# Kernel optimization log

Measured on AMD Instinct MI355X. Metric: run time of the kernel, lower is better.

The kernel has to match this reference:

```python
import jax, jax.numpy as jnp
import numpy as np

N_HEAD = 16


def setup_inputs() -> dict:
    key = jax.random.key(0)
    k1, k2, k3 = jax.random.split(key, 3)
    B, T, C = 2, 2048, 1024
    x = jax.random.normal(k1, (B, T, C), dtype=jnp.float32)
    attention_mask = jnp.zeros((B, 1, 1, T), dtype=jnp.float32)
    W_attn = jax.random.normal(k2, (C, 3 * C), dtype=jnp.float32) * 0.02
    b_attn = jnp.zeros((3 * C,), dtype=jnp.float32)
    W_proj = jax.random.normal(k3, (C, C), dtype=jnp.float32) * 0.02
    b_proj = jnp.zeros((C,), dtype=jnp.float32)
    return {"x": x, "attention_mask": attention_mask, "W_attn": W_attn,
            "b_attn": b_attn, "W_proj": W_proj, "b_proj": b_proj}


def reference(x, attention_mask, W_attn, b_attn, W_proj, b_proj):
    B, T, C = x.shape
    H = N_HEAD
    d = C // H
    qkv = x @ W_attn + b_attn                      # [B, T, 3C]
    q, k, v = jnp.split(qkv, 3, axis=-1)
    q = q.reshape(B, T, H, d).transpose(0, 2, 1, 3)  # [B, H, T, d]
    k = k.reshape(B, T, H, d).transpose(0, 2, 1, 3)
    v = v.reshape(B, T, H, d).transpose(0, 2, 1, 3)
    att = jnp.einsum('bhtd,bhsd->bhts', q, k) * (1.0 / np.sqrt(d))
    causal = jnp.tril(jnp.ones((T, T), dtype=bool))
    att = jnp.where(causal[None, None], att, jnp.float32(-10000.0))
    att = att + attention_mask                     # additive broadcast mask
    att = jax.nn.softmax(att, axis=-1)             # dropout p=0.0 -> identity
    y = jnp.einsum('bhts,bhsd->bhtd', att, v)      # [B, H, T, d]
    y = y.transpose(0, 2, 1, 3).reshape(B, T, C)
    return y @ W_proj + b_proj
```

## Files before the change

### kernel.cpp

```cpp
#include <hip/hip_runtime.h>
#include <hip/hip_bf16.h>
#include <stdint.h>

#define BATCH 2
#define TT 2048
#define CC 1024
#define NH 16
#define HD 64

typedef __attribute__((ext_vector_type(8))) short short8;
typedef __attribute__((ext_vector_type(4))) short sh4;
typedef __attribute__((ext_vector_type(4))) float f32x4;
typedef __attribute__((ext_vector_type(2))) unsigned uint2v;

#define MFMA16 __builtin_amdgcn_mfma_f32_16x16x32_bf16
#define LOG2E 1.4426950408889634f

#if defined(__has_builtin)
#if __has_builtin(__builtin_amdgcn_exp2f)
#define EXP2(x) __builtin_amdgcn_exp2f(x)
#else
#define EXP2(x) __expf((x) * 0.6931471805599453f)
#endif
#else
#define EXP2(x) __expf((x) * 0.6931471805599453f)
#endif

__device__ __forceinline__ short f2bf(float f) {
  union { float f; unsigned u; } x;
  x.f = f;
  unsigned r = x.u + 0x7FFFu + ((x.u >> 16) & 1u);
  return (short)(r >> 16);
}

__device__ __forceinline__ void transpose_cast_tile(
    const float* __restrict__ W, short* __restrict__ Wt, int K, int N,
    int n0, int k0, int tid) {
  __shared__ __align__(16) float Ls[64][68];
  {
    const int r = tid >> 4, c4 = (tid & 15) * 4;
#pragma unroll
    for (int p = 0; p < 4; ++p) {
      const float4 v = *reinterpret_cast<const float4*>(
          &W[(size_t)(k0 + r + p * 16) * N + n0 + c4]);
      *reinterpret_cast<float4*>(&Ls[r + p * 16][c4]) = v;
    }
  }
  __syncthreads();
  {
    const int n = tid >> 2;
    const int kk0 = (tid & 3) * 16;
#pragma unroll
    for (int half = 0; half < 2; ++half) {
      short8 o;
#pragma unroll
      for (int t = 0; t < 8; ++t) o[t] = f2bf(Ls[kk0 + half * 8 + t][n]);
      *reinterpret_cast<short8*>(&Wt[(size_t)(n0 + n) * K + k0 + kk0 + half * 8]) = o;
    }
  }
}

__global__ __launch_bounds__(256) void prep_fused(
    const float* __restrict__ x, short* __restrict__ xb,
    const float* __restrict__ W_attn, short* __restrict__ wat,
    const float* __restrict__ W_proj, short* __restrict__ wpt) {
  const int blk = blockIdx.x;
  const int tid = threadIdx.x;
  if (blk < 2048) {
    const int i = (blk * 256 + tid) * 8;
    const float4 a = *reinterpret_cast<const float4*>(&x[i]);
    const float4 b = *reinterpret_cast<const float4*>(&x[i + 4]);
    short8 o;
    o[0] = f2bf(a.x); o[1] = f2bf(a.y); o[2] = f2bf(a.z); o[3] = f2bf(a.w);
    o[4] = f2bf(b.x); o[5] = f2bf(b.y); o[6] = f2bf(b.z); o[7] = f2bf(b.w);
    *reinterpret_cast<short8*>(&xb[i]) = o;
  } else if (blk < 2816) {
    const int b2 = blk - 2048;
    transpose_cast_tile(W_attn, wat, CC, 3 * CC, (b2 % 48) * 64,
                        (b2 / 48) * 64, tid);
  } else {
    const int b3 = blk - 2816;
    transpose_cast_tile(W_proj, wpt, CC, CC, (b3 % 16) * 64, (b3 / 16) * 64,
                        tid);
  }
}

template <bool OUT_BF16>
__device__ __forceinline__ void gemm_bt_body(
    const short* __restrict__ A, const short* __restrict__ Bt,
    const float* __restrict__ bias, void* __restrict__ C,
    short* __restrict__ vT, int M, int N, int K, int QS) {
  __shared__ __align__(16) short SM[24576];
  short* As = SM;
  short* Bs = SM + 8192;
  const int tid = threadIdx.x;
  const int w = tid >> 6, lane = tid & 63;
  const int quad = lane >> 4, l15 = lane & 15;
  const int m0 = blockIdx.y * 64, n0 = blockIdx.x * 128;

  f32x4 acc[4][2] = {};
  const int row16 = lane >> 2;
  const int c4 = (lane & 3) * 8;

  const int rbaseA = __builtin_amdgcn_readfirstlane(w * 16);
  const int rbaseB0 = __builtin_amdgcn_readfirstlane(w * 2 * 16);
  const int rbaseB1 = __builtin_amdgcn_readfirstlane((w * 2 + 1) * 16);

#define STAGE_TILE(buf, k0)                                                    \
  {                                                                            \
    _Pragma("unroll") for (int kh = 0; kh < 2; ++kh) {                         \
      const short* ga =                                                        \
          &A[(size_t)(m0 + rbaseA + row16) * K + (k0) + kh * 32 + c4];         \
      __builtin_amdgcn_global_load_lds(                                        \
          (const __attribute__((address_space(1))) void*)ga,                   \
          (__attribute__((address_space(3))) void*)                            \
              &As[(buf)*4096 + kh * 2048 + rbaseA * 32],                       \
          16, 0, 0);                                                           \
      const short* gb0 =                                                       \
          &Bt[(size_t)(n0 + rbaseB0 + row16) * K + (k0) + kh * 32 + c4];       \
      __builtin_amdgcn_global_load_lds(                                        \
          (const __attribute__((address_space(1))) void*)gb0,                  \
          (__attribute__((address_space(3))) void*)                            \
              &Bs[(buf)*8192 + kh * 4096 + rbaseB0 * 32],                      \
          16, 0, 0);                                                           \
      const short* gb1 =                                                       \
          &Bt[(size_t)(n0 + rbaseB1 + row16) * K + (k0) + kh * 32 + c4];       \
      __builtin_amdgcn_global_load_lds(                                        \
          (const __attribute__((address_space(1))) void*)gb1,                  \
          (__attribute__((address_space(3))) void*)                            \
              &Bs[(buf)*8192 + kh * 4096 + rbaseB1 * 32],                      \
          16, 0, 0);                                                           \
    }                                                                          \
  }

  STAGE_TILE(0, 0)
  __syncthreads();

  int cur = 0;
  for (int k0 = 0; k0 < K; k0 += 64) {
    if (k0 + 64 < K) STAGE_TILE(cur ^ 1, k0 + 64)

    short8 af[2][4], bfr[2][2];
#pragma unroll
    for (int kh = 0; kh < 2; ++kh) {
#pragma unroll
      for (int i = 0; i < 4; ++i)
        af[kh][i] = *reinterpret_cast<const short8*>(
            &As[cur * 4096 + kh * 2048 + (i * 16 + l15) * 32 + quad * 8]);
#pragma unroll
      for (int j = 0; j < 2; ++j)
        bfr[kh][j] = *reinterpret_cast<const short8*>(
            &Bs[cur * 8192 + kh * 4096 + (w * 32 + j * 16 + l15) * 32 +
                quad * 8]);
    }
#pragma unroll
    for (int kh = 0; kh < 2; ++kh)
#pragma unroll
      for (int i = 0; i < 4; ++i)
#pragma unroll
        for (int j = 0; j < 2; ++j)
          acc[i][j] = MFMA16(af[kh][i], bfr[kh][j], acc[i][j], 0, 0, 0);

    __syncthreads();
    cur ^= 1;
  }
#undef STAGE_TILE

  if (OUT_BF16 && vT != nullptr && n0 >= 2 * CC) {
    const int n0v = n0 - 2 * CC;
    const int b = m0 >> 11;
    const int s_batch = m0 & (TT - 1);
    short* Ls = SM;
#pragma unroll
    for (int i = 0; i < 4; ++i) {
#pragma unroll
      for (int j = 0; j < 2; ++j) {
        const int dl = w * 32 + j * 16 + l15;
        const int sl = i * 16 + quad * 4;
        const float bb = bias[n0 + dl];
        sh4 pw;
#pragma unroll
        for (int r = 0; r < 4; ++r) pw[r] = f2bf(acc[i][j][r] + bb);
        *reinterpret_cast<sh4*>(&Ls[dl * 88 + sl]) = pw;
      }
    }
    __syncthreads();
    {
      const int row = tid >> 1, seg = tid & 1;
      const int bh = b * 16 + (n0v >> 6) + (row >> 6);
      const int d = row & 63;
      const short8* src = reinterpret_cast<const short8*>(&Ls[row * 88 + seg * 32]);
      short8* dst = reinterpret_cast<short8*>(
          &vT[((size_t)(bh * HD + d)) * TT + s_batch + seg * 32]);
#pragma unroll
      for (int t = 0; t < 4; ++t) dst[t] = src[t];
    }
    return;
  }

#pragma unroll
  for (int i = 0; i < 4; ++i) {
#pragma unroll
    for (int r = 0; r < 4; ++r) {
      const int row = m0 + i * 16 + quad * 4 + r;
#pragma unroll
      for (int j = 0; j < 2; ++j) {
        const int col = n0 + w * 32 + j * 16 + l15;
        float v = acc[i][j][r] + bias[col];
        if (col < QS) v *= 0.18033688011112042f;
        if (OUT_BF16)
          ((short*)C)[(size_t)row * N + col] = f2bf(v);
        else
          ((float*)C)[(size_t)row * N + col] = v;
      }
    }
  }
}

__global__ __launch_bounds__(256) void gemm_qkv(
    const short* __restrict__ A, const short* __restrict__ Bt,
    const float* __restrict__ bias, void* __restrict__ C,
    short* __restrict__ vT, int M, int N, int K, int QS) {
  gemm_bt_body<true>(A, Bt, bias, C, vT, M, N, K, QS);
}

__global__ __launch_bounds__(256) void gemm_proj(
    const short* __restrict__ A, const short* __restrict__ Bt,
    const float* __restrict__ bias, void* __restrict__ C, int M, int N,
    int K) {
  gemm_bt_body<false>(A, Bt, bias, C, nullptr, M, N, K, 0);
}

#define PST 72
__global__ __launch_bounds__(256) void attn_mfma8(
    const short* __restrict__ qkv, const short* __restrict__ vT,
    const float* __restrict__ mask, short* __restrict__ y) {
  __shared__ __align__(16) short Ks[2][64 * PST];
  __shared__ __align__(16) short Vs[2][64 * PST];
  __shared__ __align__(16) short Ps[64 * PST];
  const int tid = threadIdx.x;
  const int w = tid >> 6, lane = tid & 63;
  const int quad = lane >> 4, l15 = lane & 15;
  const int bh = blockIdx.y, b = bh >> 4, h = bh & 15;
  const int px = blockIdx.x;
  const int qh = 31 - px;
  const int nth = qh + 1;
  const int ntot = nth + px + 1;
  const int RS = 3 * CC;

  int qt = qh;
  int qrow0 = qt * 64 + w * 16;

  short8 qf0, qf1;
  {
    const size_t qrow = (size_t)(b * TT + qrow0 + l15) * RS + h * HD + quad * 8;
    qf0 = *reinterpret_cast<const short8*>(&qkv[qrow]);
    qf1 = *reinterpret_cast<const short8*>(&qkv[qrow + 32]);
  }

  float l_run = 0.f;
  f32x4 o_acc[4] = {};

  const int sr = tid >> 3, sc = (tid & 7) * 8;
  const short* kbase = qkv + (size_t)(b * TT + sr) * RS + CC + h * HD + sc;
  const short* vbase = vT + (size_t)(bh * HD + sr) * TT + sc;
  const float* mptr = mask + b * TT + quad * 4;
  short* psrow = &Ps[(w * 16 + l15) * PST];
  const int kfo0 = quad * 8, kfo1 = 32 + quad * 8;

  short8 kpre0 = *reinterpret_cast<const short8*>(kbase);
  short8 kpre1 = *reinterpret_cast<const short8*>(kbase + (size_t)32 * RS);
  short8 vpre0 = *reinterpret_cast<const short8*>(vbase);
  short8 vpre1 = *reinterpret_cast<const short8*>(vbase + 32 * TT);

  for (int it = 0; it < ntot; ++it) {
    const int kt = (it < nth) ? it : it - nth;
    const int s0 = kt * 64;

    f32x4 mv[4];
#pragma unroll
    for (int j = 0; j < 4; ++j)
      mv[j] = *reinterpret_cast<const f32x4*>(&mptr[s0 + j * 16]);

    if (it == nth) {
#pragma unroll
      for (int r = 0; r < 4; ++r) {
        const float lr = __shfl(l_run, quad * 4 + r, 64);
        const float inv = 1.0f / lr;
        const size_t row = (size_t)(b * TT + qrow0 + quad * 4 + r);
#pragma unroll
        for (int t = 0; t < 4; ++t)
          y[row * CC + h * HD + t * 16 + l15] = f2bf(o_acc[t][r] * inv);
      }
      qt = px;
      qrow0 = qt * 64 + w * 16;
      const size_t qrow = (size_t)(b * TT + qrow0 + l15) * RS + h * HD + quad * 8;
      qf0 = *reinterpret_cast<const short8*>(&qkv[qrow]);
      qf1 = *reinterpret_cast<const short8*>(&qkv[qrow + 32]);
      l_run = 0.f;
#pragma unroll
      for (int t = 0; t < 4; ++t) o_acc[t] = f32x4{0.f, 0.f, 0.f, 0.f};
    }

    const int cur = it & 1;
    *reinterpret_cast<short8*>(&Ks[cur][sr * PST + sc]) = kpre0;
    *reinterpret_cast<short8*>(&Ks[cur][(sr + 32) * PST + sc]) = kpre1;
    *reinterpret_cast<short8*>(&Vs[cur][sr * PST + sc]) = vpre0;
    *reinterpret_cast<short8*>(&Vs[cur][(sr + 32) * PST + sc]) = vpre1;
    __syncthreads();

    if (it + 1 < ntot) {
      const int ktn = (it + 1 == nth) ? 0 : kt + 1;
      const short* kp = kbase + (size_t)ktn * 64 * RS;
      const short* vp = vbase + ktn * 64;
      kpre0 = *reinterpret_cast<const short8*>(kp);
      kpre1 = *reinterpret_cast<const short8*>(kp + (size_t)32 * RS);
      vpre0 = *reinterpret_cast<const short8*>(vp);
      vpre1 = *reinterpret_cast<const short8*>(vp + 32 * TT);
    }

    f32x4 sa[4] = {};
#pragma unroll
    for (int j = 0; j < 4; ++j) {
      const short8 kf0 = *reinterpret_cast<const short8*>(
          &Ks[cur][(j * 16 + l15) * PST + kfo0]);
      const short8 kf1 = *reinterpret_cast<const short8*>(
          &Ks[cur][(j * 16 + l15) * PST + kfo1]);
      sa[j] = MFMA16(kf0, qf0, sa[j], 0, 0, 0);
      sa[j] = MFMA16(kf1, qf1, sa[j], 0, 0, 0);
    }

    float rs = 0.f;
    const bool boundary = (kt == qt);
    const int qg = qrow0 + l15;
#pragma unroll
    for (int j = 0; j < 4; ++j) {
      float pv[4];
#pragma unroll
      for (int r = 0; r < 4; ++r) {
        float v = __builtin_fmaf(mv[j][r], LOG2E, sa[j][r]);
        if (boundary) {
          const int sg = s0 + j * 16 + quad * 4 + r;
          if (sg > qg) v = -10000.0f;
        }
        pv[r] = EXP2(v);
      }
      union { __hip_bfloat162 h2[2]; uint2v u; } pk;
      pk.h2[0] = __float22bfloat162_rn(make_float2(pv[0], pv[1]));
      pk.h2[1] = __float22bfloat162_rn(make_float2(pv[2], pv[3]));
      *reinterpret_cast<uint2v*>(&psrow[j * 16 + quad * 4]) = pk.u;
      rs += (pv[0] + pv[1]) + (pv[2] + pv[3]);
    }
    rs += __shfl_xor(rs, 16, 64);
    rs += __shfl_xor(rs, 32, 64);
    l_run += rs;

    const short8 pf0 = *reinterpret_cast<const short8*>(&psrow[kfo0]);
    const short8 pf1 = *reinterpret_cast<const short8*>(&psrow[kfo1]);
#pragma unroll
    for (int t = 0; t < 4; ++t) {
      const short8 vf0 = *reinterpret_cast<const short8*>(
          &Vs[cur][(t * 16 + l15) * PST + kfo0]);
      const short8 vf1 = *reinterpret_cast<const short8*>(
          &Vs[cur][(t * 16 + l15) * PST + kfo1]);
      o_acc[t] = MFMA16(pf0, vf0, o_acc[t], 0, 0, 0);
      o_acc[t] = MFMA16(pf1, vf1, o_acc[t], 0, 0, 0);
    }
  }

#pragma unroll
  for (int r = 0; r < 4; ++r) {
    const float lr = __shfl(l_run, quad * 4 + r, 64);
    const float inv = 1.0f / lr;
    const size_t row = (size_t)(b * TT + qrow0 + quad * 4 + r);
#pragma unroll
    for (int t = 0; t < 4; ++t)
      y[row * CC + h * HD + t * 16 + l15] = f2bf(o_acc[t][r] * inv);
  }
}

extern "C" void kernel_launch(void* const* d_in, const int* in_sizes, int n_in,
                              void* d_out, int out_size, void* d_ws,
                              size_t ws_size, hipStream_t stream) {
  const float* x = (const float*)d_in[0];
  const float* attn_mask = (const float*)d_in[1];
  const float* W_attn = (const float*)d_in[2];
  const float* b_attn = (const float*)d_in[3];
  const float* W_proj = (const float*)d_in[4];
  const float* b_proj = (const float*)d_in[5];
  float* out = (float*)d_out;

  const int M = BATCH * TT;

  short* xb = (short*)d_ws;
  short* wat = xb + (size_t)M * CC;
  short* wpt = wat + (size_t)(3 * CC) * CC;
  short* qkvb = wpt + (size_t)CC * CC;
  short* yb = qkvb + (size_t)M * 3 * CC;
  short* vTb = yb + (size_t)M * CC;

  prep_fused<<<3072, 256, 0, stream>>>(x, xb, W_attn, wat, W_proj, wpt);

  gemm_qkv<<<dim3((3 * CC) / 128, M / 64), 256, 0, stream>>>(
      xb, wat, b_attn, qkvb, vTb, M, 3 * CC, CC, CC);

  attn_mfma8<<<dim3(16, BATCH * NH), 256, 0, stream>>>(
      qkvb, vTb, attn_mask, yb);

  gemm_proj<<<dim3(CC / 128, M / 64), 256, 0, stream>>>(
      yb, wpt, b_proj, out, M, CC, CC);
}
```

Before: 184.0 us.

## Factor additive mask into V scaling and compute softmax denominator via MFMA

The additive attention mask is rewritten as a multiplicative factor exp(mask) that scales V rows when the QKV GEMM writes V transposed, which removes the per-element mask FMA and global mask loads from the attention inner loop. The softmax row sum is now produced by an extra MFMA of P against a bf16 copy of exp(mask), replacing the shuffle reductions. The grid is also transposed so that blocks are ordered by batch-head first. This adds a small prep step and bf16 rounding of the mask factors, and it can overflow or lose precision for large mask magnitudes, since the code no longer subtracts a running max.

```diff
diff --git a/kernel.cpp b/kernel.cpp
--- a/kernel.cpp
+++ b/kernel.cpp
@@ -63,7 +63,9 @@
 __global__ __launch_bounds__(256) void prep_fused(
     const float* __restrict__ x, short* __restrict__ xb,
     const float* __restrict__ W_attn, short* __restrict__ wat,
-    const float* __restrict__ W_proj, short* __restrict__ wpt) {
+    const float* __restrict__ W_proj, short* __restrict__ wpt,
+    const float* __restrict__ mask, short* __restrict__ cb16,
+    float* __restrict__ cf32) {
   const int blk = blockIdx.x;
   const int tid = threadIdx.x;
   if (blk < 2048) {
@@ -78,10 +80,22 @@
     const int b2 = blk - 2048;
     transpose_cast_tile(W_attn, wat, CC, 3 * CC, (b2 % 48) * 64,
                         (b2 / 48) * 64, tid);
-  } else {
+  } else if (blk < 3072) {
     const int b3 = blk - 2816;
     transpose_cast_tile(W_proj, wpt, CC, CC, (b3 % 16) * 64, (b3 / 16) * 64,
                         tid);
+  } else {
+    const int b = blk - 3072;
+    const int s = tid * 8;
+    float c[8];
+#pragma unroll
+    for (int t = 0; t < 8; ++t) c[t] = __expf(mask[b * TT + s + t]);
+    short8 o;
+#pragma unroll
+    for (int t = 0; t < 8; ++t) o[t] = f2bf(c[t]);
+    *reinterpret_cast<short8*>(&cb16[b * TT + s]) = o;
+#pragma unroll
+    for (int t = 0; t < 8; ++t) cf32[b * TT + s + t] = c[t];
   }
 }
 
@@ -89,7 +103,8 @@
 __device__ __forceinline__ void gemm_bt_body(
     const short* __restrict__ A, const short* __restrict__ Bt,
     const float* __restrict__ bias, void* __restrict__ C,
-    short* __restrict__ vT, int M, int N, int K, int QS) {
+    short* __restrict__ vT, const float* __restrict__ cV, int M, int N, int K,
+    int QS) {
   __shared__ __align__(16) short SM[24576];
   short* As = SM;
   short* Bs = SM + 8192;
@@ -173,14 +188,17 @@
     short* Ls = SM;
 #pragma unroll
     for (int i = 0; i < 4; ++i) {
+      const int sl = i * 16 + quad * 4;
+      const float4 cv = *reinterpret_cast<const float4*>(&cV[m0 + sl]);
+      const float cvr[4] = {cv.x, cv.y, cv.z, cv.w};
 #pragma unroll
       for (int j = 0; j < 2; ++j) {
         const int dl = w * 32 + j * 16 + l15;
-        const int sl = i * 16 + quad * 4;
         const float bb = bias[n0 + dl];
         sh4 pw;
 #pragma unroll
-        for (int r = 0; r < 4; ++r) pw[r] = f2bf(acc[i][j][r] + bb);
+        for (int r = 0; r < 4; ++r)
+          pw[r] = f2bf((acc[i][j][r] + bb) * cvr[r]);
         *reinterpret_cast<sh4*>(&Ls[dl * 88 + sl]) = pw;
       }
     }
@@ -220,29 +238,31 @@
 __global__ __launch_bounds__(256) void gemm_qkv(
     const short* __restrict__ A, const short* __restrict__ Bt,
     const float* __restrict__ bias, void* __restrict__ C,
-    short* __restrict__ vT, int M, int N, int K, int QS) {
-  gemm_bt_body<true>(A, Bt, bias, C, vT, M, N, K, QS);
+    short* __restrict__ vT, const float* __restrict__ cV, int M, int N, int K,
+    int QS) {
+  gemm_bt_body<true>(A, Bt, bias, C, vT, cV, M, N, K, QS);
 }
 
 __global__ __launch_bounds__(256) void gemm_proj(
     const short* __restrict__ A, const short* __restrict__ Bt,
     const float* __restrict__ bias, void* __restrict__ C, int M, int N,
     int K) {
-  gemm_bt_body<false>(A, Bt, bias, C, nullptr, M, N, K, 0);
+  gemm_bt_body<false>(A, Bt, bias, C, nullptr, nullptr, M, N, K, 0);
 }
 
 #define PST 72
-__global__ __launch_bounds__(256) void attn_mfma8(
+__global__ __launch_bounds__(256) void attn_mfma10(
     const short* __restrict__ qkv, const short* __restrict__ vT,
-    const float* __restrict__ mask, short* __restrict__ y) {
+    const short* __restrict__ cb16, short* __restrict__ y) {
   __shared__ __align__(16) short Ks[2][64 * PST];
   __shared__ __align__(16) short Vs[2][64 * PST];
   __shared__ __align__(16) short Ps[64 * PST];
+  __shared__ __align__(16) short Cs[2][64];
   const int tid = threadIdx.x;
   const int w = tid >> 6, lane = tid & 63;
   const int quad = lane >> 4, l15 = lane & 15;
-  const int bh = blockIdx.y, b = bh >> 4, h = bh & 15;
-  const int px = blockIdx.x;
+  const int bh = blockIdx.x, b = bh >> 4, h = bh & 15;
+  const int px = blockIdx.y;
   const int qh = 31 - px;
   const int nth = qh + 1;
   const int ntot = nth + px + 1;
@@ -258,13 +278,13 @@
     qf1 = *reinterpret_cast<const short8*>(&qkv[qrow + 32]);
   }
 
-  float l_run = 0.f;
+  f32x4 l_acc = {};
   f32x4 o_acc[4] = {};
 
   const int sr = tid >> 3, sc = (tid & 7) * 8;
   const short* kbase = qkv + (size_t)(b * TT + sr) * RS + CC + h * HD + sc;
   const short* vbase = vT + (size_t)(bh * HD + sr) * TT + sc;
-  const float* mptr = mask + b * TT + quad * 4;
+  const short* cbase = cb16 + b * TT;
   short* psrow = &Ps[(w * 16 + l15) * PST];
   const int kfo0 = quad * 8, kfo1 = 32 + quad * 8;
 
@@ -272,21 +292,17 @@
   short8 kpre1 = *reinterpret_cast<const short8*>(kbase + (size_t)32 * RS);
   short8 vpre0 = *reinterpret_cast<const short8*>(vbase);
   short8 vpre1 = *reinterpret_cast<const short8*>(vbase + 32 * TT);
+  short8 cpre = {};
+  if (tid < 8) cpre = *reinterpret_cast<const short8*>(&cbase[tid * 8]);
 
   for (int it = 0; it < ntot; ++it) {
     const int kt = (it < nth) ? it : it - nth;
     const int s0 = kt * 64;
 
-    f32x4 mv[4];
-#pragma unroll
-    for (int j = 0; j < 4; ++j)
-      mv[j] = *reinterpret_cast<const f32x4*>(&mptr[s0 + j * 16]);
-
     if (it == nth) {
 #pragma unroll
       for (int r = 0; r < 4; ++r) {
-        const float lr = __shfl(l_run, quad * 4 + r, 64);
-        const float inv = 1.0f / lr;
+        const float inv = 1.0f / l_acc[r];
         const size_t row = (size_t)(b * TT + qrow0 + quad * 4 + r);
 #pragma unroll
         for (int t = 0; t < 4; ++t)
@@ -297,7 +313,7 @@
       const size_t qrow = (size_t)(b * TT + qrow0 + l15) * RS + h * HD + quad * 8;
       qf0 = *reinterpret_cast<const short8*>(&qkv[qrow]);
       qf1 = *reinterpret_cast<const short8*>(&qkv[qrow + 32]);
-      l_run = 0.f;
+      l_acc = f32x4{0.f, 0.f, 0.f, 0.f};
 #pragma unroll
       for (int t = 0; t < 4; ++t) o_acc[t] = f32x4{0.f, 0.f, 0.f, 0.f};
     }
@@ -307,6 +323,7 @@
     *reinterpret_cast<short8*>(&Ks[cur][(sr + 32) * PST + sc]) = kpre1;
     *reinterpret_cast<short8*>(&Vs[cur][sr * PST + sc]) = vpre0;
     *reinterpret_cast<short8*>(&Vs[cur][(sr + 32) * PST + sc]) = vpre1;
+    if (tid < 8) *reinterpret_cast<short8*>(&Cs[cur][tid * 8]) = cpre;
     __syncthreads();
 
     if (it + 1 < ntot) {
@@ -317,6 +334,8 @@
       kpre1 = *reinterpret_cast<const short8*>(kp + (size_t)32 * RS);
       vpre0 = *reinterpret_cast<const short8*>(vp);
       vpre1 = *reinterpret_cast<const short8*>(vp + 32 * TT);
+      if (tid < 8)
+        cpre = *reinterpret_cast<const short8*>(&cbase[ktn * 64 + tid * 8]);
     }
 
     f32x4 sa[4] = {};
@@ -330,7 +349,6 @@
       sa[j] = MFMA16(kf1, qf1, sa[j], 0, 0, 0);
     }
 
-    float rs = 0.f;
     const bool boundary = (kt == qt);
     const int qg = qrow0 + l15;
 #pragma unroll
@@ -338,7 +356,7 @@
       float pv[4];
 #pragma unroll
       for (int r = 0; r < 4; ++r) {
-        float v = __builtin_fmaf(mv[j][r], LOG2E, sa[j][r]);
+        float v = sa[j][r];
         if (boundary) {
           const int sg = s0 + j * 16 + quad * 4 + r;
           if (sg > qg) v = -10000.0f;
@@ -349,14 +367,14 @@
       pk.h2[0] = __float22bfloat162_rn(make_float2(pv[0], pv[1]));
       pk.h2[1] = __float22bfloat162_rn(make_float2(pv[2], pv[3]));
       *reinterpret_cast<uint2v*>(&psrow[j * 16 + quad * 4]) = pk.u;
-      rs += (pv[0] + pv[1]) + (pv[2] + pv[3]);
-    }
-    rs += __shfl_xor(rs, 16, 64);
-    rs += __shfl_xor(rs, 32, 64);
-    l_run += rs;
+    }
 
     const short8 pf0 = *reinterpret_cast<const short8*>(&psrow[kfo0]);
     const short8 pf1 = *reinterpret_cast<const short8*>(&psrow[kfo1]);
+    const short8 cf0 = *reinterpret_cast<const short8*>(&Cs[cur][kfo0]);
+    const short8 cf1 = *reinterpret_cast<const short8*>(&Cs[cur][kfo1]);
+    l_acc = MFMA16(pf0, cf0, l_acc, 0, 0, 0);
+    l_acc = MFMA16(pf1, cf1, l_acc, 0, 0, 0);
 #pragma unroll
     for (int t = 0; t < 4; ++t) {
       const short8 vf0 = *reinterpret_cast<const short8*>(
@@ -370,8 +388,7 @@
 
 #pragma unroll
   for (int r = 0; r < 4; ++r) {
-    const float lr = __shfl(l_run, quad * 4 + r, 64);
-    const float inv = 1.0f / lr;
+    const float inv = 1.0f / l_acc[r];
     const size_t row = (size_t)(b * TT + qrow0 + quad * 4 + r);
 #pragma unroll
     for (int t = 0; t < 4; ++t)
@@ -398,14 +415,17 @@
   short* qkvb = wpt + (size_t)CC * CC;
   short* yb = qkvb + (size_t)M * 3 * CC;
   short* vTb = yb + (size_t)M * CC;
-
-  prep_fused<<<3072, 256, 0, stream>>>(x, xb, W_attn, wat, W_proj, wpt);
+  short* cb16 = vTb + (size_t)BATCH * NH * HD * TT;
+  float* cf32 = (float*)(cb16 + (size_t)BATCH * TT);
+
+  prep_fused<<<3074, 256, 0, stream>>>(x, xb, W_attn, wat, W_proj, wpt,
+                                       attn_mask, cb16, cf32);
 
   gemm_qkv<<<dim3((3 * CC) / 128, M / 64), 256, 0, stream>>>(
-      xb, wat, b_attn, qkvb, vTb, M, 3 * CC, CC, CC);
-
-  attn_mfma8<<<dim3(16, BATCH * NH), 256, 0, stream>>>(
-      qkvb, vTb, attn_mask, yb);
+      xb, wat, b_attn, qkvb, vTb, cf32, M, 3 * CC, CC, CC);
+
+  attn_mfma10<<<dim3(BATCH * NH, 16), 256, 0, stream>>>(
+      qkvb, vTb, cb16, yb);
 
   gemm_proj<<<dim3(CC / 128, M / 64), 256, 0, stream>>>(
       yb, wpt, b_proj, out, M, CC, CC);
```

Measured after the change: 181.7 us. Within noise of the previous version (-1.2%).
